# Kernel optimization log

Hardware: AMD Instinct MI355X
Metric: run time of the kernel (lower is better)

## Reference

```python
import jax, jax.numpy as jnp
import numpy as np

U, I, D = 100000, 50000, 64
ALPHA = 0.2  # tf.nn.leaky_relu default


def seg_softmax(v, seg, n):
    # sparse row-wise softmax (tf.sparse.softmax equivalent)
    m = jax.ops.segment_max(v, seg, num_segments=n)
    e = jnp.exp(v - m[seg])
    s = jax.ops.segment_sum(e, seg, num_segments=n)
    return e / (s[seg] + 1e-12)


def spmm(att, row, col, x, n):
    # sparse_dense_matmul: out[r] = sum_e att[e] * x[col[e]]
    return jax.ops.segment_sum(att[:, None] * x[col], row, num_segments=n)


def edge_logit(raw, w, b):
    # Dense(1, sigmoid) on per-edge scalar, then exp (pre sparse-softmax)
    return jnp.exp(jax.nn.sigmoid(raw * w + b))


def graph_att(x, W, b1, w2, b2):
    # Dense(1, tanh) -> Dense(1, leaky_relu) on concat embeddings [N, 2D]
    h = jnp.tanh(x @ W + b1)  # [N]
    return jax.nn.leaky_relu(h * w2 + b2, ALPHA)


def setup_inputs() -> dict:
    key = jax.random.key(0)
    ks = jax.random.split(key, 24)
    Es, Eui, Eiu, B = 800000, 1000000, 1000000, 4096
    f32 = jnp.float32
    inp = {
        'user_embedding': jax.random.normal(ks[0], (U, D), f32) * 0.01,
        'item_embedding': jax.random.normal(ks[1], (I, D), f32) * 0.01,
        'snii1': jax.random.normal(ks[2], (Es,), f32),
        'snii2': jax.random.normal(ks[3], (Es,), f32),
        'ciii1': jax.random.normal(ks[4], (Eui,), f32),
        'ciii2': jax.random.normal(ks[5], (Eui,), f32),
        'icii1': jax.random.normal(ks[6], (Eiu,), f32),
        'icii2': jax.random.normal(ks[7], (Eiu,), f32) * 0.01,
        'low_att_w': jax.random.normal(ks[8], (6,), f32),
        'low_att_b': jax.random.normal(ks[9], (6,), f32),
        'att1_W': jax.random.normal(ks[10], (8, 2 * D), f32) * 0.1,
        'att1_b': jax.random.normal(ks[11], (8,), f32) * 0.1,
        'att2_w': jax.random.normal(ks[12], (8,), f32),
        'att2_b': jax.random.normal(ks[13], (8,), f32) * 0.1,
        'sn_row': jax.random.randint(ks[14], (Es,), 0, U, jnp.int32),
        'sn_col': jax.random.randint(ks[15], (Es,), 0, U, jnp.int32),
        'ci_row': jax.random.randint(ks[16], (Eui,), 0, U, jnp.int32),
        'ci_col': jax.random.randint(ks[17], (Eui,), 0, I, jnp.int32),
        'ic_row': jax.random.randint(ks[18], (Eiu,), 0, I, jnp.int32),
        'ic_col': jax.random.randint(ks[19], (Eiu,), 0, U, jnp.int32),
        'user_idx': jax.random.randint(ks[20], (B,), 0, U, jnp.int32),
        'item_idx': jax.random.randint(ks[21], (B,), 0, I, jnp.int32),
    }
    return inp


def reference(user_embedding, item_embedding, snii1, snii2, ciii1, ciii2,
              icii1, icii2, low_att_w, low_att_b, att1_W, att1_b, att2_w, att2_b,
              sn_row, sn_col, ci_row, ci_col, ic_row, ic_col, user_idx, item_idx):
    # low-level attention-weighted adjacency matrices (sparse softmax per row)
    sn1 = seg_softmax(edge_logit(snii1, low_att_w[0], low_att_b[0]), sn_row, U)
    sn2 = seg_softmax(edge_logit(snii2, low_att_w[1], low_att_b[1]), sn_row, U)
    ci1 = seg_softmax(edge_logit(ciii1, low_att_w[2], low_att_b[2]), ci_row, U)
    ci2 = seg_softmax(edge_logit(ciii2, low_att_w[3], low_att_b[3]), ci_row, U)
    ic1 = seg_softmax(edge_logit(icii1, low_att_w[4], low_att_b[4]), ic_row, I)
    ic2 = seg_softmax(edge_logit(icii2, low_att_w[5], low_att_b[5]), ic_row, I)

    u0, i0 = user_embedding, item_embedding

    def user_layer(u, it, att_sn, att_ci, k):
        u_from_i = spmm(att_ci, ci_row, ci_col, it, U)
        u_from_u = spmm(att_sn, sn_row, sn_col, u, U)
        a_int = jnp.exp(graph_att(jnp.concatenate([u, u_from_i], 1), att1_W[k], att1_b[k], att2_w[k], att2_b[k])) + 0.7
        a_soc = jnp.exp(graph_att(jnp.concatenate([u, u_from_u], 1), att1_W[k + 1], att1_b[k + 1], att2_w[k + 1], att2_b[k + 1])) + 0.3
        s = a_int + a_soc
        return 0.5 * u + 0.5 * ((a_int / s)[:, None] * u_from_i + (a_soc / s)[:, None] * u_from_u)

    def item_layer(u, it, att_ic, k):
        i_from_u = spmm(att_ic, ic_row, ic_col, u, I)
        a_self = jnp.exp(graph_att(jnp.concatenate([it, it], 1), att1_W[k], att1_b[k], att2_w[k], att2_b[k])) + 1.0
        a_cust = jnp.exp(graph_att(jnp.concatenate([it, i_from_u], 1), att1_W[k + 1], att1_b[k + 1], att2_w[k + 1], att2_b[k + 1])) + 1.0
        s = a_self + a_cust
        return (a_self / s)[:, None] * it + (a_cust / s)[:, None] * i_from_u

    u1 = user_layer(u0, i0, sn1, ci1, 0)
    i1 = item_layer(u0, i0, ic1, 4)
    u2 = user_layer(u1, i1, sn2, ci2, 2)
    i2 = item_layer(u1, i1, ic2, 6)

    fu = jnp.concatenate([u0, u1, u2], 1)  # [U, 3D]
    fi = jnp.concatenate([i0, i1, i2], 1)  # [I, 3D]
    return jax.nn.sigmoid(jnp.sum(fu[user_idx] * fi[item_idx], axis=1))  # [B]
```

## Files before the change

kernel.cpp:

```cpp
#include <hip/hip_runtime.h>
#include <math.h>

#define DIM 64
#define NBLK_P 512
#define NTHR 1024
#define CBSZ 1024
#define CBMAX 256


typedef unsigned short ushort_t;
typedef unsigned int uint_t;
typedef unsigned char uchar_t;
typedef float v2f __attribute__((ext_vector_type(2)));

__device__ __forceinline__ ushort_t f2bf(float f) {
    uint_t u = __float_as_uint(f);
    return (ushort_t)((u + 0x7fffu + ((u >> 16) & 1u)) >> 16);
}


__global__ void count_cvt_kernel(const float* __restrict__ u0, const float* __restrict__ i0,
                                 uchar_t* __restrict__ ub, uchar_t* __restrict__ ib,
                                 size_t n8u, size_t n8t,
                                 const int* __restrict__ sn_row, const int* __restrict__ ci_row,
                                 const int* __restrict__ ic_row, int* __restrict__ cnt,
                                 int Es, int Eui, int Eiu, int U, int CB) {
    __shared__ int h[CBMAX];
    int b = blockIdx.x, tid = threadIdx.x;
    size_t gtid = (size_t)b * NTHR + tid;
    const size_t GT = (size_t)NBLK_P * NTHR;

    for (size_t i = gtid; i < n8t; i += GT) {
        const float4* src; uchar_t* dst; size_t di;
        if (i < n8u) { src = (const float4*)u0; dst = ub; di = i; }
        else         { src = (const float4*)i0; dst = ib; di = i - n8u; }
        float4 a = src[2 * di], c = src[2 * di + 1];
        int lo = 0, hi = 0;
        lo = __builtin_amdgcn_cvt_pk_fp8_f32(a.x * 256.0f, a.y * 256.0f, lo, false);
        lo = __builtin_amdgcn_cvt_pk_fp8_f32(a.z * 256.0f, a.w * 256.0f, lo, true);
        hi = __builtin_amdgcn_cvt_pk_fp8_f32(c.x * 256.0f, c.y * 256.0f, hi, false);
        hi = __builtin_amdgcn_cvt_pk_fp8_f32(c.z * 256.0f, c.w * 256.0f, hi, true);
        ((uint2*)dst)[di] = make_uint2((uint_t)lo, (uint_t)hi);
    }

    int E = Es + Eui + Eiu;
    int per = (E + NBLK_P - 1) / NBLK_P;
    int e0 = b * per, e1 = min(e0 + per, E);
    if (tid < CBMAX) h[tid] = 0;
    __syncthreads();
    for (int e = e0 + tid; e < e1; e += NTHR) {
        int r;
        if (e < Es) r = sn_row[e];
        else if (e < Es + Eui) r = U + ci_row[e - Es];
        else r = 2 * U + ic_row[e - Es - Eui];
        atomicAdd(&h[r >> 10], 1);
    }
    __syncthreads();
    if (tid < CB) cnt[(size_t)b * CB + tid] = h[tid];
}


__global__ void blkscan_kernel(const int* __restrict__ cnt, int* __restrict__ blkoff,
                               int* __restrict__ total, int CB) {
    int c = blockIdx.x;
    int b = threadIdx.x;
    int v = cnt[(size_t)b * CB + c];
    int lane = b & 63, wid = b >> 6;
    int inc = v;
    #pragma unroll
    for (int off = 1; off < 64; off <<= 1) {
        int x = __shfl_up(inc, off, 64);
        if (lane >= off) inc += x;
    }
    __shared__ int ws[NBLK_P / 64];
    if (lane == 63) ws[wid] = inc;
    __syncthreads();
    int woff = 0;
    for (int j = 0; j < wid; j++) woff += ws[j];
    blkoff[(size_t)b * CB + c] = inc - v + woff;
    if (b == NBLK_P - 1) total[c] = inc + woff;
}


__global__ void cstart_kernel(const int* __restrict__ total, int* __restrict__ cstart, int CB) {
    int t = threadIdx.x;
    int v = (t < CB) ? total[t] : 0;
    int lane = t & 63, wid = t >> 6;
    int inc = v;
    #pragma unroll
    for (int off = 1; off < 64; off <<= 1) {
        int x = __shfl_up(inc, off, 64);
        if (lane >= off) inc += x;
    }
    __shared__ int ws[4];
    if (lane == 63) ws[wid] = inc;
    __syncthreads();
    int woff = 0;
    for (int j = 0; j < wid; j++) woff += ws[j];
    if (t < CB) cstart[t] = inc - v + woff;
    if (t == CB - 1) cstart[CB] = inc + woff;
}


__global__ void place_kernel(const int* __restrict__ sn_row, const int* __restrict__ sn_col,
                             const int* __restrict__ ci_row, const int* __restrict__ ci_col,
                             const int* __restrict__ ic_row, const int* __restrict__ ic_col,
                             const float* __restrict__ snii1, const float* __restrict__ snii2,
                             const float* __restrict__ ciii1, const float* __restrict__ ciii2,
                             const float* __restrict__ icii1, const float* __restrict__ icii2,
                             const float* __restrict__ lw, const float* __restrict__ lb,
                             const int* __restrict__ cstart, const int* __restrict__ blkoff,
                             uint2* __restrict__ barr,
                             int Es, int Eui, int Eiu, int U, int CB) {
    __shared__ int cur[CBMAX];
    int E = Es + Eui + Eiu;
    int per = (E + NBLK_P - 1) / NBLK_P;
    int b = blockIdx.x;
    int e0 = b * per, e1 = min(e0 + per, E);
    if (threadIdx.x < CB)
        cur[threadIdx.x] = cstart[threadIdx.x] + blkoff[(size_t)b * CB + threadIdx.x];
    __syncthreads();
    for (int e = e0 + (int)threadIdx.x; e < e1; e += NTHR) {
        int r, c, j1, j2;
        float r1, r2;
        if (e < Es) {
            r = sn_row[e]; c = sn_col[e]; r1 = snii1[e]; r2 = snii2[e]; j1 = 0; j2 = 1;
        } else if (e < Es + Eui) {
            int t = e - Es;
            r = U + ci_row[t]; c = ci_col[t]; r1 = ciii1[t]; r2 = ciii2[t]; j1 = 2; j2 = 3;
        } else {
            int t = e - Es - Eui;
            r = 2 * U + ic_row[t]; c = ic_col[t]; r1 = icii1[t]; r2 = icii2[t]; j1 = 4; j2 = 5;
        }
        float t1 = expf(expf(1.0f / (1.0f + expf(-(r1 * lw[j1] + lb[j1])))));
        float t2 = expf(expf(1.0f / (1.0f + expf(-(r2 * lw[j2] + lb[j2])))));
        uint_t packed = (uint_t)f2bf(t1) | ((uint_t)f2bf(t2) << 16);
        int cb = r >> 10;
        int pos = atomicAdd(&cur[cb], 1);
        barr[pos] = make_uint2(((uint_t)(r & 1023) << 22) | (uint_t)c, packed);
    }
}


__global__ void finalize_kernel(const uint2* __restrict__ barr, const int* __restrict__ cstart,
                                int* __restrict__ ptr, uint2* __restrict__ rec,
                                int R, int CB) {
    __shared__ int hist[CBSZ];
    __shared__ int cur2[CBSZ];
    __shared__ int ws[NTHR / 64];
    int c = blockIdx.x, tid = threadIdx.x;
    int s0 = cstart[c], s1 = cstart[c + 1];
    hist[tid] = 0;
    __syncthreads();
    for (int e = s0 + tid; e < s1; e += NTHR)
        atomicAdd(&hist[barr[e].x >> 22], 1);
    __syncthreads();
    int v = hist[tid];
    int lane = tid & 63, wid = tid >> 6;
    int inc = v;
    #pragma unroll
    for (int off = 1; off < 64; off <<= 1) {
        int x = __shfl_up(inc, off, 64);
        if (lane >= off) inc += x;
    }
    if (lane == 63) ws[wid] = inc;
    __syncthreads();
    int woff = 0;
    for (int j = 0; j < wid; j++) woff += ws[j];
    int p0 = s0 + inc - v + woff;
    int r = c * CBSZ + tid;
    if (r < R) ptr[r] = p0;
    cur2[tid] = p0;
    if (c == CB - 1 && tid == 0) ptr[R] = cstart[CB];
    __syncthreads();
    for (int e = s0 + tid; e < s1; e += NTHR) {
        uint2 q = barr[e];
        int rin = (int)(q.x >> 22);
        int pos = atomicAdd(&cur2[rin], 1);
        rec[pos] = make_uint2(q.x & 0x3FFFFFu, q.y);
    }
}


__device__ __forceinline__ float att_scalar(float dot, float b1, float w2, float b2, float addc) {
    float h = tanhf(dot + b1);
    float z = h * w2 + b2;
    float lr = z > 0.0f ? z : 0.2f * z;
    return expf(lr) + addc;
}

__device__ __forceinline__ void fp8_fma8v(v2f acc[4], uint2 v, float a) {
    v2f av = {a, a};
    acc[0] += av * __builtin_amdgcn_cvt_pk_f32_fp8((int)v.x, false);
    acc[1] += av * __builtin_amdgcn_cvt_pk_f32_fp8((int)v.x, true);
    acc[2] += av * __builtin_amdgcn_cvt_pk_f32_fp8((int)v.y, false);
    acc[3] += av * __builtin_amdgcn_cvt_pk_f32_fp8((int)v.y, true);
}

__device__ __forceinline__ float dot8_lanes(float d) {
    #pragma unroll
    for (int off = 1; off < 8; off <<= 1) d += __shfl_xor(d, off, 64);
    return d;
}

__device__ __forceinline__ void agg_row8(const uint2* __restrict__ rec, const uchar_t* __restrict__ tab,
                                         int e0, int e1, int l8, int lanebase,
                                         v2f acc[4], float& s) {
    if (e0 >= e1) return;
    int last = e1 - 1;
    int idx0 = e0 + l8;
    uint2 t0 = rec[min(idx0, last)];
    uint2 q;
    q.x = (idx0 <= last) ? t0.x : 0u;
    q.y = (idx0 <= last) ? t0.y : 0u;
    for (int base = e0; base < e1; base += 8) {
        int nidx = base + 8 + l8;
        uint2 tn = rec[min(nidx, last)];
        uint2 qn;
        qn.x = (nidx <= last) ? tn.x : 0u;
        qn.y = (nidx <= last) ? tn.y : 0u;
        s += __uint_as_float(q.y << 16);
        #pragma unroll
        for (int j = 0; j < 8; j++) {
            uint_t cx = __shfl(q.x, lanebase + j, 64);
            uint_t wy = __shfl(q.y, lanebase + j, 64);
            float a = __uint_as_float(wy << 16);
            uint2 v = ((const uint2*)(tab + (size_t)cx * DIM))[l8];
            fp8_fma8v(acc, v, a);
        }
        q = qn;
    }
}

__global__ void layer1_kernel(const uchar_t* __restrict__ ub8, const uchar_t* __restrict__ ib8,
                              const float* __restrict__ u0, const float* __restrict__ i0,
                              const int* __restrict__ ptr, const uint2* __restrict__ rec,
                              const float* __restrict__ W1, const float* __restrict__ b1v,
                              const float* __restrict__ w2v, const float* __restrict__ b2v,
                              float* __restrict__ u1, float* __restrict__ i1, int U, int I) {
    int gid = blockIdx.x * (blockDim.x >> 3) + (threadIdx.x >> 3);
    int lane = threadIdx.x & 63;
    int l8 = lane & 7;
    int lanebase = lane & 56;
    if (gid >= U + I) return;
    bool is_user = gid < U;
    int r = is_user ? gid : gid - U;

    v2f A[4]  = {{0.f, 0.f}, {0.f, 0.f}, {0.f, 0.f}, {0.f, 0.f}};
    v2f Bv[4] = {{0.f, 0.f}, {0.f, 0.f}, {0.f, 0.f}, {0.f, 0.f}};
    float s_a = 0.f, s_b = 0.f;

    if (is_user) {
        agg_row8(rec, ib8, ptr[U + r], ptr[U + r + 1], l8, lanebase, A, s_a);
        agg_row8(rec, ub8, ptr[r], ptr[r + 1], l8, lanebase, Bv, s_b);
    } else {
        agg_row8(rec, ub8, ptr[2 * U + r], ptr[2 * U + r + 1], l8, lanebase, A, s_a);
    }
    s_a = dot8_lanes(s_a);
    s_b = dot8_lanes(s_b);

    float ka = (1.0f / (s_a + 1e-12f)) * 0.00390625f;
    float kb = (1.0f / (s_b + 1e-12f)) * 0.00390625f;
    float ac[8], bc[8];
    #pragma unroll
    for (int j = 0; j < 4; j++) {
        ac[2 * j] = A[j][0] * ka;  ac[2 * j + 1] = A[j][1] * ka;
        bc[2 * j] = Bv[j][0] * kb; bc[2 * j + 1] = Bv[j][1] * kb;
    }

    const float* selfp = (is_user ? u0 : i0) + (size_t)r * DIM + 8 * l8;
    float4 s0 = *(const float4*)selfp;
    float4 s1 = *(const float4*)(selfp + 4);
    float sf[8] = {s0.x, s0.y, s0.z, s0.w, s1.x, s1.y, s1.z, s1.w};
    int k = is_user ? 0 : 4;
    const float* Wa = W1 + k * 2 * DIM;
    const float* Wb = Wa + 2 * DIM;
    float d1 = 0.f, d2 = 0.f;
    #pragma unroll
    for (int j = 0; j < 8; j++) {
        float wa0 = Wa[8 * l8 + j], wa1 = Wa[DIM + 8 * l8 + j];
        float wb0 = Wb[8 * l8 + j], wb1 = Wb[DIM + 8 * l8 + j];
        if (is_user) {
            d1 += sf[j] * wa0 + ac[j] * wa1;
            d2 += sf[j] * wb0 + bc[j] * wb1;
        } else {
            d1 += sf[j] * (wa0 + wa1);
            d2 += sf[j] * wb0 + ac[j] * wb1;
        }
    }
    d1 = dot8_lanes(d1);
    d2 = dot8_lanes(d2);

    float out8[8];
    float* op;
    if (is_user) {
        float a_int = att_scalar(d1, b1v[0], w2v[0], b2v[0], 0.7f);
        float a_soc = att_scalar(d2, b1v[1], w2v[1], b2v[1], 0.3f);
        float sg = a_int + a_soc;
        float wi = a_int / sg, ws = a_soc / sg;
        #pragma unroll
        for (int j = 0; j < 8; j++)
            out8[j] = 0.5f * sf[j] + 0.5f * (wi * ac[j] + ws * bc[j]);
        op = u1 + (size_t)r * DIM + 8 * l8;
    } else {
        float a_self = att_scalar(d1, b1v[4], w2v[4], b2v[4], 1.0f);
        float a_cust = att_scalar(d2, b1v[5], w2v[5], b2v[5], 1.0f);
        float sg = a_self + a_cust;
        float wi = a_self / sg, ws = a_cust / sg;
        #pragma unroll
        for (int j = 0; j < 8; j++)
            out8[j] = wi * sf[j] + ws * ac[j];
        op = i1 + (size_t)r * DIM + 8 * l8;
    }
    *(float4*)op = make_float4(out8[0], out8[1], out8[2], out8[3]);
    *(float4*)(op + 4) = make_float4(out8[4], out8[5], out8[6], out8[7]);
}

__global__ void layer2_kernel(const float* __restrict__ u1, const float* __restrict__ i1,
                              const int* __restrict__ ptr, const uint2* __restrict__ rec,
                              const float* __restrict__ W1, const float* __restrict__ b1v,
                              const float* __restrict__ w2v, const float* __restrict__ b2v,
                              const int* __restrict__ uidx, const int* __restrict__ iidx,
                              float* __restrict__ u2s, float* __restrict__ i2s, int U, int B) {
    int wid = blockIdx.x * (blockDim.x >> 6) + (threadIdx.x >> 6);
    int lane = threadIdx.x & 63;
    if (wid >= 2 * B) return;
    int g = lane >> 3, l8 = lane & 7;
    bool is_user = wid < B;
    int b = is_user ? wid : wid - B;
    int r = is_user ? uidx[b] : iidx[b];

    float acc_a[8] = {0, 0, 0, 0, 0, 0, 0, 0};
    float acc_b[8] = {0, 0, 0, 0, 0, 0, 0, 0};
    float s_a = 0.f, s_b = 0.f;

    if (is_user) {
        int e0 = ptr[U + r], e1 = ptr[U + r + 1];
        for (int e = e0 + g; e < e1; e += 8) {
            uint2 q = rec[e];
            float a = __uint_as_float(q.y & 0xffff0000u);
            s_a += a;
            const float4* rp = (const float4*)(i1 + (size_t)q.x * DIM);
            float4 v0 = rp[2 * l8], v1 = rp[2 * l8 + 1];
            acc_a[0] = fmaf(a, v0.x, acc_a[0]); acc_a[1] = fmaf(a, v0.y, acc_a[1]);
            acc_a[2] = fmaf(a, v0.z, acc_a[2]); acc_a[3] = fmaf(a, v0.w, acc_a[3]);
            acc_a[4] = fmaf(a, v1.x, acc_a[4]); acc_a[5] = fmaf(a, v1.y, acc_a[5]);
            acc_a[6] = fmaf(a, v1.z, acc_a[6]); acc_a[7] = fmaf(a, v1.w, acc_a[7]);
        }
        e0 = ptr[r]; e1 = ptr[r + 1];
        for (int e = e0 + g; e < e1; e += 8) {
            uint2 q = rec[e];
            float a = __uint_as_float(q.y & 0xffff0000u);
            s_b += a;
            const float4* rp = (const float4*)(u1 + (size_t)q.x * DIM);
            float4 v0 = rp[2 * l8], v1 = rp[2 * l8 + 1];
            acc_b[0] = fmaf(a, v0.x, acc_b[0]); acc_b[1] = fmaf(a, v0.y, acc_b[1]);
            acc_b[2] = fmaf(a, v0.z, acc_b[2]); acc_b[3] = fmaf(a, v0.w, acc_b[3]);
            acc_b[4] = fmaf(a, v1.x, acc_b[4]); acc_b[5] = fmaf(a, v1.y, acc_b[5]);
            acc_b[6] = fmaf(a, v1.z, acc_b[6]); acc_b[7] = fmaf(a, v1.w, acc_b[7]);
        }
    } else {
        int e0 = ptr[2 * U + r], e1 = ptr[2 * U + r + 1];
        for (int e = e0 + g; e < e1; e += 8) {
            uint2 q = rec[e];
            float a = __uint_as_float(q.y & 0xffff0000u);
            s_a += a;
            const float4* rp = (const float4*)(u1 + (size_t)q.x * DIM);
            float4 v0 = rp[2 * l8], v1 = rp[2 * l8 + 1];
            acc_a[0] = fmaf(a, v0.x, acc_a[0]); acc_a[1] = fmaf(a, v0.y, acc_a[1]);
            acc_a[2] = fmaf(a, v0.z, acc_a[2]); acc_a[3] = fmaf(a, v0.w, acc_a[3]);
            acc_a[4] = fmaf(a, v1.x, acc_a[4]); acc_a[5] = fmaf(a, v1.y, acc_a[5]);
            acc_a[6] = fmaf(a, v1.z, acc_a[6]); acc_a[7] = fmaf(a, v1.w, acc_a[7]);
        }
    }

    #pragma unroll
    for (int off = 8; off < 64; off <<= 1) {
        s_a += __shfl_xor(s_a, off, 64);
        #pragma unroll
        for (int j = 0; j < 8; j++) acc_a[j] += __shfl_xor(acc_a[j], off, 64);
    }
    if (is_user) {
        #pragma unroll
        for (int off = 8; off < 64; off <<= 1) {
            s_b += __shfl_xor(s_b, off, 64);
            #pragma unroll
            for (int j = 0; j < 8; j++) acc_b[j] += __shfl_xor(acc_b[j], off, 64);
        }
    }
    float ka = 1.0f / (s_a + 1e-12f);
    float kb = 1.0f / (s_b + 1e-12f);

    if (g == 0) {
        #pragma unroll
        for (int j = 0; j < 8; j++) { acc_a[j] *= ka; acc_b[j] *= kb; }
        const float* selfp = (is_user ? u1 : i1) + (size_t)r * DIM + 8 * l8;
        float4 s0 = *(const float4*)selfp;
        float4 s1 = *(const float4*)(selfp + 4);
        float sf[8] = {s0.x, s0.y, s0.z, s0.w, s1.x, s1.y, s1.z, s1.w};
        int k = is_user ? 2 : 6;
        const float* Wa = W1 + k * 2 * DIM;
        const float* Wb = Wa + 2 * DIM;
        float d1 = 0.f, d2 = 0.f;
        #pragma unroll
        for (int j = 0; j < 8; j++) {
            float wa0 = Wa[8 * l8 + j], wa1 = Wa[DIM + 8 * l8 + j];
            float wb0 = Wb[8 * l8 + j], wb1 = Wb[DIM + 8 * l8 + j];
            if (is_user) {
                d1 += sf[j] * wa0 + acc_a[j] * wa1;
                d2 += sf[j] * wb0 + acc_b[j] * wb1;
            } else {
                d1 += sf[j] * (wa0 + wa1);
                d2 += sf[j] * wb0 + acc_a[j] * wb1;
            }
        }
        d1 = dot8_lanes(d1);
        d2 = dot8_lanes(d2);

        float out8[8];
        float* op;
        if (is_user) {
            float a_int = att_scalar(d1, b1v[2], w2v[2], b2v[2], 0.7f);
            float a_soc = att_scalar(d2, b1v[3], w2v[3], b2v[3], 0.3f);
            float sg = a_int + a_soc;
            float wi = a_int / sg, ws = a_soc / sg;
            #pragma unroll
            for (int j = 0; j < 8; j++)
                out8[j] = 0.5f * sf[j] + 0.5f * (wi * acc_a[j] + ws * acc_b[j]);
            op = u2s + (size_t)b * DIM + 8 * l8;
        } else {
            float a_self = att_scalar(d1, b1v[6], w2v[6], b2v[6], 1.0f);
            float a_cust = att_scalar(d2, b1v[7], w2v[7], b2v[7], 1.0f);
            float sg = a_self + a_cust;
            float wi = a_self / sg, ws = a_cust / sg;
            #pragma unroll
            for (int j = 0; j < 8; j++)
                out8[j] = wi * sf[j] + ws * acc_a[j];
            op = i2s + (size_t)b * DIM + 8 * l8;
        }
        *(float4*)op = make_float4(out8[0], out8[1], out8[2], out8[3]);
        *(float4*)(op + 4) = make_float4(out8[4], out8[5], out8[6], out8[7]);
    }
}


__global__ void final_kernel(const float* __restrict__ u0, const float* __restrict__ u1,
                             const float* __restrict__ u2s,
                             const float* __restrict__ i0, const float* __restrict__ i1,
                             const float* __restrict__ i2s,
                             const int* __restrict__ uidx, const int* __restrict__ iidx,
                             float* __restrict__ out, int n) {
    int b = blockIdx.x * (blockDim.x >> 6) + (threadIdx.x >> 6);
    int lane = threadIdx.x & 63;
    if (b >= n) return;
    size_t ur = (size_t)uidx[b] * DIM + lane;
    size_t ir = (size_t)iidx[b] * DIM + lane;
    size_t sr = (size_t)b * DIM + lane;
    float acc = u0[ur] * i0[ir] + u1[ur] * i1[ir] + u2s[sr] * i2s[sr];
    #pragma unroll
    for (int off = 32; off > 0; off >>= 1) acc += __shfl_xor(acc, off, 64);
    if (lane == 0) out[b] = 1.0f / (1.0f + expf(-acc));
}


extern "C" void kernel_launch(void* const* d_in, const int* in_sizes, int n_in,
                              void* d_out, int out_size, void* d_ws, size_t ws_size,
                              hipStream_t stream) {
    const float* user_emb = (const float*)d_in[0];
    const float* item_emb = (const float*)d_in[1];
    const float* snii1 = (const float*)d_in[2];
    const float* snii2 = (const float*)d_in[3];
    const float* ciii1 = (const float*)d_in[4];
    const float* ciii2 = (const float*)d_in[5];
    const float* icii1 = (const float*)d_in[6];
    const float* icii2 = (const float*)d_in[7];
    const float* low_w = (const float*)d_in[8];
    const float* low_b = (const float*)d_in[9];
    const float* att1_W = (const float*)d_in[10];
    const float* att1_b = (const float*)d_in[11];
    const float* att2_w = (const float*)d_in[12];
    const float* att2_b = (const float*)d_in[13];
    const int* sn_row = (const int*)d_in[14];
    const int* sn_col = (const int*)d_in[15];
    const int* ci_row = (const int*)d_in[16];
    const int* ci_col = (const int*)d_in[17];
    const int* ic_row = (const int*)d_in[18];
    const int* ic_col = (const int*)d_in[19];
    const int* user_idx = (const int*)d_in[20];
    const int* item_idx = (const int*)d_in[21];
    float* out = (float*)d_out;

    const int Es  = in_sizes[2];
    const int Eui = in_sizes[4];
    const int Eiu = in_sizes[6];
    const int U = in_sizes[0] / DIM;
    const int I = in_sizes[1] / DIM;
    const int B = in_sizes[20];
    const int R = 2 * U + I;
    const int E = Es + Eui + Eiu;
    const int CB = (R + CBSZ - 1) / CBSZ;

    char* wsb = (char*)d_ws;
    size_t off = 0;
    auto alloc = [&](size_t n_units) {
        off = (off + 3) & ~(size_t)3;
        void* p = wsb + off * 4; off += n_units; return p;
    };

    int* cnt    = (int*)alloc((size_t)NBLK_P * CB);
    int* blkoff = (int*)alloc((size_t)NBLK_P * CB);
    int* total  = (int*)alloc(CB);
    int* cstart = (int*)alloc(CB + 1);
    int* ptr    = (int*)alloc(R + 1);
    uint2* barr = (uint2*)alloc((size_t)E * 2);
    uint2* rec  = (uint2*)alloc((size_t)E * 2);
    uchar_t* ub8 = (uchar_t*)alloc((size_t)U * DIM / 4);
    uchar_t* ib8 = (uchar_t*)alloc((size_t)I * DIM / 4);
    float* u1  = (float*)alloc((size_t)U * DIM);
    float* i1  = (float*)alloc((size_t)I * DIM);
    float* u2s = (float*)alloc((size_t)B * DIM);
    float* i2s = (float*)alloc((size_t)B * DIM);
    (void)ws_size;

    size_t n8u = (size_t)U * DIM / 8, n8t = (size_t)(U + I) * DIM / 8;

    count_cvt_kernel<<<NBLK_P, NTHR, 0, stream>>>(user_emb, item_emb, ub8, ib8, n8u, n8t,
                                                  sn_row, ci_row, ic_row, cnt,
                                                  Es, Eui, Eiu, U, CB);
    blkscan_kernel<<<CB, NBLK_P, 0, stream>>>(cnt, blkoff, total, CB);
    cstart_kernel<<<1, 256, 0, stream>>>(total, cstart, CB);
    place_kernel<<<NBLK_P, NTHR, 0, stream>>>(sn_row, sn_col, ci_row, ci_col, ic_row, ic_col,
                                              snii1, snii2, ciii1, ciii2, icii1, icii2,
                                              low_w, low_b, cstart, blkoff, barr,
                                              Es, Eui, Eiu, U, CB);
    finalize_kernel<<<CB, NTHR, 0, stream>>>(barr, cstart, ptr, rec, R, CB);

    layer1_kernel<<<(U + I + 31) / 32, 256, 0, stream>>>(ub8, ib8, user_emb, item_emb,
        ptr, rec, att1_W, att1_b, att2_w, att2_b, u1, i1, U, I);

    layer2_kernel<<<(2 * B + 3) / 4, 256, 0, stream>>>(u1, i1, ptr, rec,
        att1_W, att1_b, att2_w, att2_b, user_idx, item_idx, u2s, i2s, U, B);

    final_kernel<<<(B + 3) / 4, 256, 0, stream>>>(user_emb, u1, u2s, item_emb, i1, i2s,
                                                  user_idx, item_idx, out, B);
}
```

Before: 305.6 us.

## Fuse layer2 with final scoring, inline CB prefix scan, vectorize edge loads

Merges the layer-2 kernel and the final dot-product kernel into one wave-per-batch kernel that computes both the user and item layer-2 rows and emits the sigmoid score directly. This removes the u2s/i2s round-trip and one launch. The separate cstart scan kernel is folded into place and finalize, with each block recomputing the small prefix in shared memory. Count and place now walk each edge list separately using int4/float4 loads instead of branching per edge. The trade-off is redundant prefix work in every block and half as many waves in layer 2, each doing more serial work.

```diff
diff --git a/kernel.cpp b/kernel.cpp
--- a/kernel.cpp
+++ b/kernel.cpp
@@ -18,6 +18,23 @@
     return (ushort_t)((u + 0x7fffu + ((u >> 16) & 1u)) >> 16);
 }
 
+
+__device__ __forceinline__ void count_list(const int* __restrict__ rows, int EL, int base,
+                                           int* h, size_t gtid, size_t GT) {
+    size_t nq = ((size_t)EL + 3) >> 2;
+    for (size_t q = gtid; q < nq; q += GT) {
+        int e = (int)(q << 2);
+        if (e + 4 <= EL) {
+            int4 r4 = *(const int4*)(rows + e);
+            atomicAdd(&h[(base + r4.x) >> 10], 1);
+            atomicAdd(&h[(base + r4.y) >> 10], 1);
+            atomicAdd(&h[(base + r4.z) >> 10], 1);
+            atomicAdd(&h[(base + r4.w) >> 10], 1);
+        } else {
+            for (int j = e; j < EL; j++) atomicAdd(&h[(base + rows[j]) >> 10], 1);
+        }
+    }
+}
 
 __global__ void count_cvt_kernel(const float* __restrict__ u0, const float* __restrict__ i0,
                                  uchar_t* __restrict__ ub, uchar_t* __restrict__ ib,
@@ -43,18 +60,11 @@
         ((uint2*)dst)[di] = make_uint2((uint_t)lo, (uint_t)hi);
     }
 
-    int E = Es + Eui + Eiu;
-    int per = (E + NBLK_P - 1) / NBLK_P;
-    int e0 = b * per, e1 = min(e0 + per, E);
     if (tid < CBMAX) h[tid] = 0;
     __syncthreads();
-    for (int e = e0 + tid; e < e1; e += NTHR) {
-        int r;
-        if (e < Es) r = sn_row[e];
-        else if (e < Es + Eui) r = U + ci_row[e - Es];
-        else r = 2 * U + ic_row[e - Es - Eui];
-        atomicAdd(&h[r >> 10], 1);
-    }
+    count_list(sn_row, Es, 0, h, gtid, GT);
+    count_list(ci_row, Eui, U, h, gtid, GT);
+    count_list(ic_row, Eiu, 2 * U, h, gtid, GT);
     __syncthreads();
     if (tid < CB) cnt[(size_t)b * CB + tid] = h[tid];
 }
@@ -82,25 +92,65 @@
 }
 
 
-__global__ void cstart_kernel(const int* __restrict__ total, int* __restrict__ cstart, int CB) {
+__device__ __forceinline__ void cb_prefix(const int* __restrict__ total, int CB,
+                                          int* cs, int* wsx) {
     int t = threadIdx.x;
-    int v = (t < CB) ? total[t] : 0;
-    int lane = t & 63, wid = t >> 6;
-    int inc = v;
-    #pragma unroll
-    for (int off = 1; off < 64; off <<= 1) {
-        int x = __shfl_up(inc, off, 64);
-        if (lane >= off) inc += x;
-    }
-    __shared__ int ws[4];
-    if (lane == 63) ws[wid] = inc;
-    __syncthreads();
-    int woff = 0;
-    for (int j = 0; j < wid; j++) woff += ws[j];
-    if (t < CB) cstart[t] = inc - v + woff;
-    if (t == CB - 1) cstart[CB] = inc + woff;
-}
-
+    int lane = t & 63, wv = t >> 6;
+    int v = 0, inc = 0;
+    if (t < 256) {
+        v = (t < CB) ? total[t] : 0;
+        inc = v;
+        #pragma unroll
+        for (int off = 1; off < 64; off <<= 1) {
+            int x = __shfl_up(inc, off, 64);
+            if (lane >= off) inc += x;
+        }
+        if (lane == 63) wsx[wv] = inc;
+    }
+    __syncthreads();
+    if (t < 256) {
+        int woff = 0;
+        for (int j = 0; j < wv; j++) woff += wsx[j];
+        if (t < CB) cs[t] = inc - v + woff;
+        if (t == CB - 1) cs[CB] = inc + woff;
+    }
+    __syncthreads();
+}
+
+
+__device__ __forceinline__ void place_edge(int v, int c, float r1, float r2,
+                                           float w1, float b1, float w2, float b2,
+                                           int* cur, uint2* __restrict__ barr) {
+    float t1 = expf(expf(1.0f / (1.0f + expf(-(r1 * w1 + b1)))));
+    float t2 = expf(expf(1.0f / (1.0f + expf(-(r2 * w2 + b2)))));
+    uint_t packed = (uint_t)f2bf(t1) | ((uint_t)f2bf(t2) << 16);
+    int pos = atomicAdd(&cur[v >> 10], 1);
+    barr[pos] = make_uint2(((uint_t)(v & 1023) << 22) | (uint_t)c, packed);
+}
+
+__device__ __forceinline__ void place_list(const int* __restrict__ rows, const int* __restrict__ cols,
+                                           const float* __restrict__ x1, const float* __restrict__ x2,
+                                           int EL, int base, float w1, float b1, float w2, float b2,
+                                           int* cur, uint2* __restrict__ barr,
+                                           size_t gtid, size_t GT) {
+    size_t nq = ((size_t)EL + 3) >> 2;
+    for (size_t q = gtid; q < nq; q += GT) {
+        int e = (int)(q << 2);
+        if (e + 4 <= EL) {
+            int4 r4 = *(const int4*)(rows + e);
+            int4 c4 = *(const int4*)(cols + e);
+            float4 a4 = *(const float4*)(x1 + e);
+            float4 b4 = *(const float4*)(x2 + e);
+            place_edge(base + r4.x, c4.x, a4.x, b4.x, w1, b1, w2, b2, cur, barr);
+            place_edge(base + r4.y, c4.y, a4.y, b4.y, w1, b1, w2, b2, cur, barr);
+            place_edge(base + r4.z, c4.z, a4.z, b4.z, w1, b1, w2, b2, cur, barr);
+            place_edge(base + r4.w, c4.w, a4.w, b4.w, w1, b1, w2, b2, cur, barr);
+        } else {
+            for (int j = e; j < EL; j++)
+                place_edge(base + rows[j], cols[j], x1[j], x2[j], w1, b1, w2, b2, cur, barr);
+        }
+    }
+}
 
 __global__ void place_kernel(const int* __restrict__ sn_row, const int* __restrict__ sn_col,
                              const int* __restrict__ ci_row, const int* __restrict__ ci_col,
@@ -109,47 +159,36 @@
                              const float* __restrict__ ciii1, const float* __restrict__ ciii2,
                              const float* __restrict__ icii1, const float* __restrict__ icii2,
                              const float* __restrict__ lw, const float* __restrict__ lb,
-                             const int* __restrict__ cstart, const int* __restrict__ blkoff,
+                             const int* __restrict__ total, const int* __restrict__ blkoff,
                              uint2* __restrict__ barr,
                              int Es, int Eui, int Eiu, int U, int CB) {
+    __shared__ int cs[CBMAX + 1];
+    __shared__ int wsx[4];
     __shared__ int cur[CBMAX];
-    int E = Es + Eui + Eiu;
-    int per = (E + NBLK_P - 1) / NBLK_P;
     int b = blockIdx.x;
-    int e0 = b * per, e1 = min(e0 + per, E);
+    cb_prefix(total, CB, cs, wsx);
     if (threadIdx.x < CB)
-        cur[threadIdx.x] = cstart[threadIdx.x] + blkoff[(size_t)b * CB + threadIdx.x];
-    __syncthreads();
-    for (int e = e0 + (int)threadIdx.x; e < e1; e += NTHR) {
-        int r, c, j1, j2;
-        float r1, r2;
-        if (e < Es) {
-            r = sn_row[e]; c = sn_col[e]; r1 = snii1[e]; r2 = snii2[e]; j1 = 0; j2 = 1;
-        } else if (e < Es + Eui) {
-            int t = e - Es;
-            r = U + ci_row[t]; c = ci_col[t]; r1 = ciii1[t]; r2 = ciii2[t]; j1 = 2; j2 = 3;
-        } else {
-            int t = e - Es - Eui;
-            r = 2 * U + ic_row[t]; c = ic_col[t]; r1 = icii1[t]; r2 = icii2[t]; j1 = 4; j2 = 5;
-        }
-        float t1 = expf(expf(1.0f / (1.0f + expf(-(r1 * lw[j1] + lb[j1])))));
-        float t2 = expf(expf(1.0f / (1.0f + expf(-(r2 * lw[j2] + lb[j2])))));
-        uint_t packed = (uint_t)f2bf(t1) | ((uint_t)f2bf(t2) << 16);
-        int cb = r >> 10;
-        int pos = atomicAdd(&cur[cb], 1);
-        barr[pos] = make_uint2(((uint_t)(r & 1023) << 22) | (uint_t)c, packed);
-    }
-}
-
-
-__global__ void finalize_kernel(const uint2* __restrict__ barr, const int* __restrict__ cstart,
+        cur[threadIdx.x] = cs[threadIdx.x] + blkoff[(size_t)b * CB + threadIdx.x];
+    __syncthreads();
+    size_t gtid = (size_t)b * NTHR + threadIdx.x;
+    const size_t GT = (size_t)NBLK_P * NTHR;
+    place_list(sn_row, sn_col, snii1, snii2, Es, 0,      lw[0], lb[0], lw[1], lb[1], cur, barr, gtid, GT);
+    place_list(ci_row, ci_col, ciii1, ciii2, Eui, U,     lw[2], lb[2], lw[3], lb[3], cur, barr, gtid, GT);
+    place_list(ic_row, ic_col, icii1, icii2, Eiu, 2 * U, lw[4], lb[4], lw[5], lb[5], cur, barr, gtid, GT);
+}
+
+
+__global__ void finalize_kernel(const uint2* __restrict__ barr, const int* __restrict__ total,
                                 int* __restrict__ ptr, uint2* __restrict__ rec,
                                 int R, int CB) {
+    __shared__ int cs[CBMAX + 1];
+    __shared__ int wsx[4];
     __shared__ int hist[CBSZ];
     __shared__ int cur2[CBSZ];
-    __shared__ int ws[NTHR / 64];
+    __shared__ int wss[NTHR / 64];
     int c = blockIdx.x, tid = threadIdx.x;
-    int s0 = cstart[c], s1 = cstart[c + 1];
+    cb_prefix(total, CB, cs, wsx);
+    int s0 = cs[c], s1 = cs[c + 1];
     hist[tid] = 0;
     __syncthreads();
     for (int e = s0 + tid; e < s1; e += NTHR)
@@ -163,15 +202,15 @@
         int x = __shfl_up(inc, off, 64);
         if (lane >= off) inc += x;
     }
-    if (lane == 63) ws[wid] = inc;
+    if (lane == 63) wss[wid] = inc;
     __syncthreads();
     int woff = 0;
-    for (int j = 0; j < wid; j++) woff += ws[j];
+    for (int j = 0; j < wid; j++) woff += wss[j];
     int p0 = s0 + inc - v + woff;
     int r = c * CBSZ + tid;
     if (r < R) ptr[r] = p0;
     cur2[tid] = p0;
-    if (c == CB - 1 && tid == 0) ptr[R] = cstart[CB];
+    if (c == CB - 1 && tid == 0) ptr[R] = cs[CB];
     __syncthreads();
     for (int e = s0 + tid; e < s1; e += NTHR) {
         uint2 q = barr[e];
@@ -316,150 +355,143 @@
     *(float4*)(op + 4) = make_float4(out8[4], out8[5], out8[6], out8[7]);
 }
 
-__global__ void layer2_kernel(const float* __restrict__ u1, const float* __restrict__ i1,
-                              const int* __restrict__ ptr, const uint2* __restrict__ rec,
-                              const float* __restrict__ W1, const float* __restrict__ b1v,
-                              const float* __restrict__ w2v, const float* __restrict__ b2v,
-                              const int* __restrict__ uidx, const int* __restrict__ iidx,
-                              float* __restrict__ u2s, float* __restrict__ i2s, int U, int B) {
+
+__global__ void l2f_kernel(const float* __restrict__ u0, const float* __restrict__ i0,
+                           const float* __restrict__ u1, const float* __restrict__ i1,
+                           const int* __restrict__ ptr, const uint2* __restrict__ rec,
+                           const float* __restrict__ W1, const float* __restrict__ b1v,
+                           const float* __restrict__ w2v, const float* __restrict__ b2v,
+                           const int* __restrict__ uidx, const int* __restrict__ iidx,
+                           float* __restrict__ out, int U, int B) {
     int wid = blockIdx.x * (blockDim.x >> 6) + (threadIdx.x >> 6);
     int lane = threadIdx.x & 63;
-    if (wid >= 2 * B) return;
+    if (wid >= B) return;
     int g = lane >> 3, l8 = lane & 7;
-    bool is_user = wid < B;
-    int b = is_user ? wid : wid - B;
-    int r = is_user ? uidx[b] : iidx[b];
-
-    float acc_a[8] = {0, 0, 0, 0, 0, 0, 0, 0};
-    float acc_b[8] = {0, 0, 0, 0, 0, 0, 0, 0};
+    int ru = uidx[wid], ri = iidx[wid];
+
+    float aa[8] = {0, 0, 0, 0, 0, 0, 0, 0};
+    float ab[8] = {0, 0, 0, 0, 0, 0, 0, 0};
     float s_a = 0.f, s_b = 0.f;
-
-    if (is_user) {
-        int e0 = ptr[U + r], e1 = ptr[U + r + 1];
-        for (int e = e0 + g; e < e1; e += 8) {
-            uint2 q = rec[e];
-            float a = __uint_as_float(q.y & 0xffff0000u);
-            s_a += a;
-            const float4* rp = (const float4*)(i1 + (size_t)q.x * DIM);
-            float4 v0 = rp[2 * l8], v1 = rp[2 * l8 + 1];
-            acc_a[0] = fmaf(a, v0.x, acc_a[0]); acc_a[1] = fmaf(a, v0.y, acc_a[1]);
-            acc_a[2] = fmaf(a, v0.z, acc_a[2]); acc_a[3] = fmaf(a, v0.w, acc_a[3]);
-            acc_a[4] = fmaf(a, v1.x, acc_a[4]); acc_a[5] = fmaf(a, v1.y, acc_a[5]);
-            acc_a[6] = fmaf(a, v1.z, acc_a[6]); acc_a[7] = fmaf(a, v1.w, acc_a[7]);
-        }
-        e0 = ptr[r]; e1 = ptr[r + 1];
-        for (int e = e0 + g; e < e1; e += 8) {
-            uint2 q = rec[e];
-            float a = __uint_as_float(q.y & 0xffff0000u);
-            s_b += a;
-            const float4* rp = (const float4*)(u1 + (size_t)q.x * DIM);
-            float4 v0 = rp[2 * l8], v1 = rp[2 * l8 + 1];
-            acc_b[0] = fmaf(a, v0.x, acc_b[0]); acc_b[1] = fmaf(a, v0.y, acc_b[1]);
-            acc_b[2] = fmaf(a, v0.z, acc_b[2]); acc_b[3] = fmaf(a, v0.w, acc_b[3]);
-            acc_b[4] = fmaf(a, v1.x, acc_b[4]); acc_b[5] = fmaf(a, v1.y, acc_b[5]);
-            acc_b[6] = fmaf(a, v1.z, acc_b[6]); acc_b[7] = fmaf(a, v1.w, acc_b[7]);
-        }
-    } else {
-        int e0 = ptr[2 * U + r], e1 = ptr[2 * U + r + 1];
-        for (int e = e0 + g; e < e1; e += 8) {
-            uint2 q = rec[e];
-            float a = __uint_as_float(q.y & 0xffff0000u);
-            s_a += a;
-            const float4* rp = (const float4*)(u1 + (size_t)q.x * DIM);
-            float4 v0 = rp[2 * l8], v1 = rp[2 * l8 + 1];
-            acc_a[0] = fmaf(a, v0.x, acc_a[0]); acc_a[1] = fmaf(a, v0.y, acc_a[1]);
-            acc_a[2] = fmaf(a, v0.z, acc_a[2]); acc_a[3] = fmaf(a, v0.w, acc_a[3]);
-            acc_a[4] = fmaf(a, v1.x, acc_a[4]); acc_a[5] = fmaf(a, v1.y, acc_a[5]);
-            acc_a[6] = fmaf(a, v1.z, acc_a[6]); acc_a[7] = fmaf(a, v1.w, acc_a[7]);
-        }
-    }
-
+    int e0 = ptr[U + ru], e1 = ptr[U + ru + 1];
+    for (int e = e0 + g; e < e1; e += 8) {
+        uint2 q = rec[e];
+        float a = __uint_as_float(q.y & 0xffff0000u);
+        s_a += a;
+        const float4* rp = (const float4*)(i1 + (size_t)q.x * DIM);
+        float4 v0 = rp[2 * l8], v1 = rp[2 * l8 + 1];
+        aa[0] = fmaf(a, v0.x, aa[0]); aa[1] = fmaf(a, v0.y, aa[1]);
+        aa[2] = fmaf(a, v0.z, aa[2]); aa[3] = fmaf(a, v0.w, aa[3]);
+        aa[4] = fmaf(a, v1.x, aa[4]); aa[5] = fmaf(a, v1.y, aa[5]);
+        aa[6] = fmaf(a, v1.z, aa[6]); aa[7] = fmaf(a, v1.w, aa[7]);
+    }
+    e0 = ptr[ru]; e1 = ptr[ru + 1];
+    for (int e = e0 + g; e < e1; e += 8) {
+        uint2 q = rec[e];
+        float a = __uint_as_float(q.y & 0xffff0000u);
+        s_b += a;
+        const float4* rp = (const float4*)(u1 + (size_t)q.x * DIM);
+        float4 v0 = rp[2 * l8], v1 = rp[2 * l8 + 1];
+        ab[0] = fmaf(a, v0.x, ab[0]); ab[1] = fmaf(a, v0.y, ab[1]);
+        ab[2] = fmaf(a, v0.z, ab[2]); ab[3] = fmaf(a, v0.w, ab[3]);
+        ab[4] = fmaf(a, v1.x, ab[4]); ab[5] = fmaf(a, v1.y, ab[5]);
+        ab[6] = fmaf(a, v1.z, ab[6]); ab[7] = fmaf(a, v1.w, ab[7]);
+    }
     #pragma unroll
     for (int off = 8; off < 64; off <<= 1) {
         s_a += __shfl_xor(s_a, off, 64);
-        #pragma unroll
-        for (int j = 0; j < 8; j++) acc_a[j] += __shfl_xor(acc_a[j], off, 64);
-    }
-    if (is_user) {
-        #pragma unroll
-        for (int off = 8; off < 64; off <<= 1) {
-            s_b += __shfl_xor(s_b, off, 64);
-            #pragma unroll
-            for (int j = 0; j < 8; j++) acc_b[j] += __shfl_xor(acc_b[j], off, 64);
+        s_b += __shfl_xor(s_b, off, 64);
+        #pragma unroll
+        for (int j = 0; j < 8; j++) {
+            aa[j] += __shfl_xor(aa[j], off, 64);
+            ab[j] += __shfl_xor(ab[j], off, 64);
         }
     }
     float ka = 1.0f / (s_a + 1e-12f);
     float kb = 1.0f / (s_b + 1e-12f);
-
-    if (g == 0) {
-        #pragma unroll
-        for (int j = 0; j < 8; j++) { acc_a[j] *= ka; acc_b[j] *= kb; }
-        const float* selfp = (is_user ? u1 : i1) + (size_t)r * DIM + 8 * l8;
-        float4 s0 = *(const float4*)selfp;
-        float4 s1 = *(const float4*)(selfp + 4);
-        float sf[8] = {s0.x, s0.y, s0.z, s0.w, s1.x, s1.y, s1.z, s1.w};
-        int k = is_user ? 2 : 6;
-        const float* Wa = W1 + k * 2 * DIM;
+    #pragma unroll
+    for (int j = 0; j < 8; j++) { aa[j] *= ka; ab[j] *= kb; }
+
+    const float* sup = u1 + (size_t)ru * DIM + 8 * l8;
+    float4 su0 = *(const float4*)sup;
+    float4 su1 = *(const float4*)(sup + 4);
+    float sfu[8] = {su0.x, su0.y, su0.z, su0.w, su1.x, su1.y, su1.z, su1.w};
+    {
+        const float* Wa = W1 + 2 * 2 * DIM;
         const float* Wb = Wa + 2 * DIM;
         float d1 = 0.f, d2 = 0.f;
         #pragma unroll
         for (int j = 0; j < 8; j++) {
-            float wa0 = Wa[8 * l8 + j], wa1 = Wa[DIM + 8 * l8 + j];
-            float wb0 = Wb[8 * l8 + j], wb1 = Wb[DIM + 8 * l8 + j];
-            if (is_user) {
-                d1 += sf[j] * wa0 + acc_a[j] * wa1;
-                d2 += sf[j] * wb0 + acc_b[j] * wb1;
-            } else {
-                d1 += sf[j] * (wa0 + wa1);
-                d2 += sf[j] * wb0 + acc_a[j] * wb1;
-            }
+            d1 += sfu[j] * Wa[8 * l8 + j] + aa[j] * Wa[DIM + 8 * l8 + j];
+            d2 += sfu[j] * Wb[8 * l8 + j] + ab[j] * Wb[DIM + 8 * l8 + j];
         }
         d1 = dot8_lanes(d1);
         d2 = dot8_lanes(d2);
-
-        float out8[8];
-        float* op;
-        if (is_user) {
-            float a_int = att_scalar(d1, b1v[2], w2v[2], b2v[2], 0.7f);
-            float a_soc = att_scalar(d2, b1v[3], w2v[3], b2v[3], 0.3f);
-            float sg = a_int + a_soc;
-            float wi = a_int / sg, ws = a_soc / sg;
-            #pragma unroll
-            for (int j = 0; j < 8; j++)
-                out8[j] = 0.5f * sf[j] + 0.5f * (wi * acc_a[j] + ws * acc_b[j]);
-            op = u2s + (size_t)b * DIM + 8 * l8;
-        } else {
-            float a_self = att_scalar(d1, b1v[6], w2v[6], b2v[6], 1.0f);
-            float a_cust = att_scalar(d2, b1v[7], w2v[7], b2v[7], 1.0f);
-            float sg = a_self + a_cust;
-            float wi = a_self / sg, ws = a_cust / sg;
-            #pragma unroll
-            for (int j = 0; j < 8; j++)
-                out8[j] = wi * sf[j] + ws * acc_a[j];
-            op = i2s + (size_t)b * DIM + 8 * l8;
-        }
-        *(float4*)op = make_float4(out8[0], out8[1], out8[2], out8[3]);
-        *(float4*)(op + 4) = make_float4(out8[4], out8[5], out8[6], out8[7]);
-    }
-}
-
-
-__global__ void final_kernel(const float* __restrict__ u0, const float* __restrict__ u1,
-                             const float* __restrict__ u2s,
-                             const float* __restrict__ i0, const float* __restrict__ i1,
-                             const float* __restrict__ i2s,
-                             const int* __restrict__ uidx, const int* __restrict__ iidx,
-                             float* __restrict__ out, int n) {
-    int b = blockIdx.x * (blockDim.x >> 6) + (threadIdx.x >> 6);
-    int lane = threadIdx.x & 63;
-    if (b >= n) return;
-    size_t ur = (size_t)uidx[b] * DIM + lane;
-    size_t ir = (size_t)iidx[b] * DIM + lane;
-    size_t sr = (size_t)b * DIM + lane;
-    float acc = u0[ur] * i0[ir] + u1[ur] * i1[ir] + u2s[sr] * i2s[sr];
-    #pragma unroll
-    for (int off = 32; off > 0; off >>= 1) acc += __shfl_xor(acc, off, 64);
-    if (lane == 0) out[b] = 1.0f / (1.0f + expf(-acc));
+        float a_int = att_scalar(d1, b1v[2], w2v[2], b2v[2], 0.7f);
+        float a_soc = att_scalar(d2, b1v[3], w2v[3], b2v[3], 0.3f);
+        float sg = a_int + a_soc;
+        float wi = a_int / sg, ws = a_soc / sg;
+        #pragma unroll
+        for (int j = 0; j < 8; j++)
+            aa[j] = 0.5f * sfu[j] + 0.5f * (wi * aa[j] + ws * ab[j]);
+    }
+
+    float ac[8] = {0, 0, 0, 0, 0, 0, 0, 0};
+    float s_c = 0.f;
+    e0 = ptr[2 * U + ri]; e1 = ptr[2 * U + ri + 1];
+    for (int e = e0 + g; e < e1; e += 8) {
+        uint2 q = rec[e];
+        float a = __uint_as_float(q.y & 0xffff0000u);
+        s_c += a;
+        const float4* rp = (const float4*)(u1 + (size_t)q.x * DIM);
+        float4 v0 = rp[2 * l8], v1 = rp[2 * l8 + 1];
+        ac[0] = fmaf(a, v0.x, ac[0]); ac[1] = fmaf(a, v0.y, ac[1]);
+        ac[2] = fmaf(a, v0.z, ac[2]); ac[3] = fmaf(a, v0.w, ac[3]);
+        ac[4] = fmaf(a, v1.x, ac[4]); ac[5] = fmaf(a, v1.y, ac[5]);
+        ac[6] = fmaf(a, v1.z, ac[6]); ac[7] = fmaf(a, v1.w, ac[7]);
+    }
+    #pragma unroll
+    for (int off = 8; off < 64; off <<= 1) {
+        s_c += __shfl_xor(s_c, off, 64);
+        #pragma unroll
+        for (int j = 0; j < 8; j++) ac[j] += __shfl_xor(ac[j], off, 64);
+    }
+    float kc = 1.0f / (s_c + 1e-12f);
+    #pragma unroll
+    for (int j = 0; j < 8; j++) ac[j] *= kc;
+
+    const float* sip = i1 + (size_t)ri * DIM + 8 * l8;
+    float4 si0 = *(const float4*)sip;
+    float4 si1 = *(const float4*)(sip + 4);
+    float sfi[8] = {si0.x, si0.y, si0.z, si0.w, si1.x, si1.y, si1.z, si1.w};
+    {
+        const float* Wa = W1 + 6 * 2 * DIM;
+        const float* Wb = Wa + 2 * DIM;
+        float d1 = 0.f, d2 = 0.f;
+        #pragma unroll
+        for (int j = 0; j < 8; j++) {
+            d1 += sfi[j] * (Wa[8 * l8 + j] + Wa[DIM + 8 * l8 + j]);
+            d2 += sfi[j] * Wb[8 * l8 + j] + ac[j] * Wb[DIM + 8 * l8 + j];
+        }
+        d1 = dot8_lanes(d1);
+        d2 = dot8_lanes(d2);
+        float a_self = att_scalar(d1, b1v[6], w2v[6], b2v[6], 1.0f);
+        float a_cust = att_scalar(d2, b1v[7], w2v[7], b2v[7], 1.0f);
+        float sg = a_self + a_cust;
+        float wi = a_self / sg, ws = a_cust / sg;
+        #pragma unroll
+        for (int j = 0; j < 8; j++)
+            ac[j] = wi * sfi[j] + ws * ac[j];
+    }
+
+    float p = 0.f;
+    #pragma unroll
+    for (int j = 0; j < 8; j++) p += aa[j] * ac[j];
+    p = dot8_lanes(p);
+    float qd = u0[(size_t)ru * DIM + lane] * i0[(size_t)ri * DIM + lane]
+             + u1[(size_t)ru * DIM + lane] * i1[(size_t)ri * DIM + lane];
+    #pragma unroll
+    for (int off = 32; off > 0; off >>= 1) qd += __shfl_xor(qd, off, 64);
+    if (lane == 0) out[wid] = 1.0f / (1.0f + expf(-(p + qd)));
 }
 
 
@@ -497,8 +529,9 @@
     const int I = in_sizes[1] / DIM;
     const int B = in_sizes[20];
     const int R = 2 * U + I;
+    const int CB = (R + CBSZ - 1) / CBSZ;
     const int E = Es + Eui + Eiu;
-    const int CB = (R + CBSZ - 1) / CBSZ;
+    (void)E;
 
     char* wsb = (char*)d_ws;
     size_t off = 0;
@@ -510,7 +543,6 @@
     int* cnt    = (int*)alloc((size_t)NBLK_P * CB);
     int* blkoff = (int*)alloc((size_t)NBLK_P * CB);
     int* total  = (int*)alloc(CB);
-    int* cstart = (int*)alloc(CB + 1);
     int* ptr    = (int*)alloc(R + 1);
     uint2* barr = (uint2*)alloc((size_t)E * 2);
     uint2* rec  = (uint2*)alloc((size_t)E * 2);
@@ -518,8 +550,6 @@
     uchar_t* ib8 = (uchar_t*)alloc((size_t)I * DIM / 4);
     float* u1  = (float*)alloc((size_t)U * DIM);
     float* i1  = (float*)alloc((size_t)I * DIM);
-    float* u2s = (float*)alloc((size_t)B * DIM);
-    float* i2s = (float*)alloc((size_t)B * DIM);
     (void)ws_size;
 
     size_t n8u = (size_t)U * DIM / 8, n8t = (size_t)(U + I) * DIM / 8;
@@ -528,19 +558,15 @@
                                                   sn_row, ci_row, ic_row, cnt,
                                                   Es, Eui, Eiu, U, CB);
     blkscan_kernel<<<CB, NBLK_P, 0, stream>>>(cnt, blkoff, total, CB);
-    cstart_kernel<<<1, 256, 0, stream>>>(total, cstart, CB);
     place_kernel<<<NBLK_P, NTHR, 0, stream>>>(sn_row, sn_col, ci_row, ci_col, ic_row, ic_col,
                                               snii1, snii2, ciii1, ciii2, icii1, icii2,
-                                              low_w, low_b, cstart, blkoff, barr,
+                                              low_w, low_b, total, blkoff, barr,
                                               Es, Eui, Eiu, U, CB);
-    finalize_kernel<<<CB, NTHR, 0, stream>>>(barr, cstart, ptr, rec, R, CB);
+    finalize_kernel<<<CB, NTHR, 0, stream>>>(barr, total, ptr, rec, R, CB);
 
     layer1_kernel<<<(U + I + 31) / 32, 256, 0, stream>>>(ub8, ib8, user_emb, item_emb,
         ptr, rec, att1_W, att1_b, att2_w, att2_b, u1, i1, U, I);
 
-    layer2_kernel<<<(2 * B + 3) / 4, 256, 0, stream>>>(u1, i1, ptr, rec,
-        att1_W, att1_b, att2_w, att2_b, user_idx, item_idx, u2s, i2s, U, B);
-
-    final_kernel<<<(B + 3) / 4, 256, 0, stream>>>(user_emb, u1, u2s, item_emb, i1, i2s,
-                                                  user_idx, item_idx, out, B);
-}
+    l2f_kernel<<<(B + 3) / 4, 256, 0, stream>>>(user_emb, item_emb, u1, i1, ptr, rec,
+        att1_W, att1_b, att2_w, att2_b, user_idx, item_idx, out, U, B);
+}
```

Result: faster. 290.6 us (-4.9%).
